# Performance work log

Hardware: AMD Instinct MI355X
Metric: run time of the kernel (lower is better)

The kernel has to match this reference:

```python
import jax, jax.numpy as jnp
import numpy as np

SIGMA = 1.0
T0, T1 = 0.0, 1.0
C, D = 8192, 3


def gram(x, y, sigma):
    # K(x, y) = exp(-||x - y||^2 / sigma^2), shape [N, M]
    x2 = jnp.sum(x * x, axis=-1)
    y2 = jnp.sum(y * y, axis=-1)
    d2 = x2[:, None] + y2[None, :] - 2.0 * (x @ y.T)
    return jnp.exp(-d2 / (sigma * sigma))


def setup_inputs() -> dict:
    key = jax.random.key(0)
    k1, k2 = jax.random.split(key)
    momentum = 0.01 * jax.random.normal(k1, (C, D), dtype=jnp.float32)
    control_points = jax.random.normal(k2, (C, D), dtype=jnp.float32)
    return {"momentum": momentum, "control_points": control_points, "steps": 5}


def reference(momentum, control_points, steps):
    sigma = SIGMA

    def hamiltonian(c, m):
        # H = 0.5 * sum(m * K(c, c) @ m)
        K = gram(c, c, sigma)
        return 0.5 * jnp.sum(m * (K @ m))

    def dyn(s):
        # Hamilton's equations: dc = dH/dm, dm = -dH/dc
        c, m = s[0], s[1]
        gc, gm = jax.grad(hamiltonian, argnums=(0, 1))(c, m)
        return jnp.stack([gm, -gc])

    t_span = jnp.linspace(T0, T1, steps)
    dt = (T1 - T0) / (steps - 1)
    s0 = jnp.stack([control_points, momentum])  # [2, C, d]

    def rk4_step(s, _):
        k1 = dyn(s)
        k2 = dyn(s + 0.5 * dt * k1)
        k3 = dyn(s + 0.5 * dt * k2)
        k4 = dyn(s + dt * k3)
        s_next = s + (dt / 6.0) * (k1 + 2.0 * k2 + 2.0 * k3 + k4)
        return s_next, s_next

    _, traj = jax.lax.scan(rk4_step, s0, None, length=steps - 1)
    st = jnp.concatenate([s0[None], traj], axis=0)  # [steps, 2, C, d]
    return t_span, st
```

## Files before the change

kernel.cpp:

```cpp
#include <hip/hip_runtime.h>


#define CN   8192
#define TPB  256
#define PTS  2
#define IGRP (TPB * PTS)
#define NIB  (CN / IGRP)
#define SJ   128
#define JC   (CN / SJ)
#define SSZ  (2 * CN * 3)

#define CSCALE 1.2011224087864498f
#define FSCALE (2.0f / CSCALE)


__global__ __launch_bounds__(TPB, 8) void dyn_kernel(
    const float* __restrict__ scur, const float* __restrict__ kprev,
    float coef, float* __restrict__ kout)
{
    __shared__ float4 jt[JC][2];
    const int tid = threadIdx.x;
    const int jbase = blockIdx.y * JC;

    {
        float* jf = (float*)jt;
#pragma unroll
        for (int q = tid; q < JC * 8; q += TPB) {
            const int p = jbase + (q >> 3), s = q & 7;
            float v = 0.f;
            if (s < 3) {
                v = (scur[p*3 + s] + coef * kprev[s*CN + p]) * CSCALE;
            } else if (s >= 4 && s < 7) {
                const int d = s - 4;
                v = scur[CN*3 + p*3 + d] + coef * kprev[(3 + d)*CN + p];
            }
            jf[q] = v;
        }
    }

    const int i0 = blockIdx.x * IGRP + tid;
    const int i1 = i0 + TPB;
    const float cx0 = (scur[i0*3+0] + coef*kprev[0*CN+i0]) * CSCALE;
    const float cy0 = (scur[i0*3+1] + coef*kprev[1*CN+i0]) * CSCALE;
    const float cz0 = (scur[i0*3+2] + coef*kprev[2*CN+i0]) * CSCALE;
    const float mx0 =  scur[CN*3+i0*3+0] + coef*kprev[3*CN+i0];
    const float my0 =  scur[CN*3+i0*3+1] + coef*kprev[4*CN+i0];
    const float mz0 =  scur[CN*3+i0*3+2] + coef*kprev[5*CN+i0];
    const float cx1 = (scur[i1*3+0] + coef*kprev[0*CN+i1]) * CSCALE;
    const float cy1 = (scur[i1*3+1] + coef*kprev[1*CN+i1]) * CSCALE;
    const float cz1 = (scur[i1*3+2] + coef*kprev[2*CN+i1]) * CSCALE;
    const float mx1 =  scur[CN*3+i1*3+0] + coef*kprev[3*CN+i1];
    const float my1 =  scur[CN*3+i1*3+1] + coef*kprev[4*CN+i1];
    const float mz1 =  scur[CN*3+i1*3+2] + coef*kprev[5*CN+i1];

    float gx0=0.f,gy0=0.f,gz0=0.f, fx0=0.f,fy0=0.f,fz0=0.f;
    float gx1=0.f,gy1=0.f,gz1=0.f, fx1=0.f,fy1=0.f,fz1=0.f;

    __syncthreads();

#pragma unroll 4
    for (int j = 0; j < JC; ++j) {
        const float4 A = jt[j][0];
        const float4 M = jt[j][1];
        {
            const float dx = cx0 - A.x, dy = cy0 - A.y, dz = cz0 - A.z;
            const float d2 = fmaf(dx, dx, fmaf(dy, dy, dz*dz));
            const float e  = __builtin_amdgcn_exp2f(-d2);
            const float md = fmaf(mx0, M.x, fmaf(my0, M.y, mz0 * M.z));
            const float w  = md * e;
            gx0 = fmaf(e, M.x, gx0); gy0 = fmaf(e, M.y, gy0); gz0 = fmaf(e, M.z, gz0);
            fx0 = fmaf(w, dx, fx0);  fy0 = fmaf(w, dy, fy0);  fz0 = fmaf(w, dz, fz0);
        }
        {
            const float dx = cx1 - A.x, dy = cy1 - A.y, dz = cz1 - A.z;
            const float d2 = fmaf(dx, dx, fmaf(dy, dy, dz*dz));
            const float e  = __builtin_amdgcn_exp2f(-d2);
            const float md = fmaf(mx1, M.x, fmaf(my1, M.y, mz1 * M.z));
            const float w  = md * e;
            gx1 = fmaf(e, M.x, gx1); gy1 = fmaf(e, M.y, gy1); gz1 = fmaf(e, M.z, gz1);
            fx1 = fmaf(w, dx, fx1);  fy1 = fmaf(w, dy, fy1);  fz1 = fmaf(w, dz, fz1);
        }
    }

    atomicAdd(&kout[0*CN+i0], gx0); atomicAdd(&kout[1*CN+i0], gy0); atomicAdd(&kout[2*CN+i0], gz0);
    atomicAdd(&kout[3*CN+i0], FSCALE*fx0); atomicAdd(&kout[4*CN+i0], FSCALE*fy0); atomicAdd(&kout[5*CN+i0], FSCALE*fz0);
    atomicAdd(&kout[0*CN+i1], gx1); atomicAdd(&kout[1*CN+i1], gy1); atomicAdd(&kout[2*CN+i1], gz1);
    atomicAdd(&kout[3*CN+i1], FSCALE*fx1); atomicAdd(&kout[4*CN+i1], FSCALE*fy1); atomicAdd(&kout[5*CN+i1], FSCALE*fz1);
}

__global__ __launch_bounds__(256) void advance_kernel(
    float* __restrict__ scur,
    float* __restrict__ k1, float* __restrict__ k2,
    float* __restrict__ k3, float* __restrict__ k4,
    float* __restrict__ outslot, float dt6)
{
    const int idx = blockIdx.x * 256 + threadIdx.x;
    if (idx >= 6 * CN) return;
    const int plane = idx >> 13, i = idx & (CN - 1);
    const int comp = (plane >= 3) ? 1 : 0, d = plane - comp * 3;
    const int off = comp * CN * 3 + i * 3 + d;
    const float v = scur[off] + dt6 * (k1[idx] + 2.f * (k2[idx] + k3[idx]) + k4[idx]);
    scur[off]    = v;
    outslot[off] = v;
    k1[idx] = 0.f; k2[idx] = 0.f; k3[idx] = 0.f; k4[idx] = 0.f;
}

__global__ __launch_bounds__(256) void init_kernel(
    const float* __restrict__ mom, const float* __restrict__ cp,
    float* __restrict__ out, float* __restrict__ scur,
    float* __restrict__ kb0, float* __restrict__ kb1,
    float* __restrict__ kb2, float* __restrict__ kb3)
{
    const int idx = blockIdx.x * 256 + threadIdx.x;
    if (idx < 5) out[idx] = 0.25f * (float)idx;
    if (idx < 6 * CN) { kb0[idx]=0.f; kb1[idx]=0.f; kb2[idx]=0.f; kb3[idx]=0.f; }
    if (idx < CN * 3) {
        const float cv = cp[idx], mv = mom[idx];
        scur[idx]          = cv;
        scur[CN * 3 + idx] = mv;
        out[5 + idx]            = cv;
        out[5 + CN * 3 + idx]   = mv;
    }
}

extern "C" void kernel_launch(void* const* d_in, const int* in_sizes, int n_in,
                              void* d_out, int out_size, void* d_ws, size_t ws_size,
                              hipStream_t stream)
{
    const float* mom = (const float*)d_in[0];
    const float* cp  = (const float*)d_in[1];
    float* out = (float*)d_out;
    float* ws  = (float*)d_ws;

    float* scur = ws;
    float* kb0  = ws + SSZ;
    float* kb1  = kb0 + 6 * CN;
    float* kb2  = kb1 + 6 * CN;
    float* kb3  = kb2 + 6 * CN;

    const float dt  = 0.25f;
    const float dt6 = dt / 6.f;

    init_kernel<<<(6 * CN + 255) / 256, 256, 0, stream>>>(mom, cp, out, scur,
                                                          kb0, kb1, kb2, kb3);
    dim3 dgrid(NIB, SJ);
    const int agrid = (6 * CN + 255) / 256;
    for (int step = 0; step < 4; ++step) {
        float* outslot = out + 5 + (size_t)(step + 1) * SSZ;
        dyn_kernel<<<dgrid, TPB, 0, stream>>>(scur, kb0, 0.0f,      kb0);
        dyn_kernel<<<dgrid, TPB, 0, stream>>>(scur, kb0, 0.5f * dt, kb1);
        dyn_kernel<<<dgrid, TPB, 0, stream>>>(scur, kb1, 0.5f * dt, kb2);
        dyn_kernel<<<dgrid, TPB, 0, stream>>>(scur, kb2, dt,        kb3);
        advance_kernel<<<agrid, 256, 0, stream>>>(scur, kb0, kb1, kb2, kb3, outslot, dt6);
    }
}
```

Baseline: 605.8 us.

## Expand distance algebraically and raise per-thread points to four

```diff
diff --git a/kernel.cpp b/kernel.cpp
--- a/kernel.cpp
+++ b/kernel.cpp
@@ -3,7 +3,7 @@
 
 #define CN   8192
 #define TPB  256
-#define PTS  2
+#define PTS  4
 #define IGRP (TPB * PTS)
 #define NIB  (CN / IGRP)
 #define SJ   128
@@ -13,8 +13,7 @@
 #define CSCALE 1.2011224087864498f
 #define FSCALE (2.0f / CSCALE)
 
-
-__global__ __launch_bounds__(TPB, 8) void dyn_kernel(
+__global__ __launch_bounds__(TPB, 4) void dyn_kernel(
     const float* __restrict__ scur, const float* __restrict__ kprev,
     float coef, float* __restrict__ kout)
 {
@@ -22,70 +21,66 @@
     const int tid = threadIdx.x;
     const int jbase = blockIdx.y * JC;
 
-    {
-        float* jf = (float*)jt;
+    if (tid < JC) {
+        const int p = jbase + tid;
+        const float sx = (scur[p*3+0] + coef * kprev[0*CN+p]) * CSCALE;
+        const float sy = (scur[p*3+1] + coef * kprev[1*CN+p]) * CSCALE;
+        const float sz = (scur[p*3+2] + coef * kprev[2*CN+p]) * CSCALE;
+        jt[tid][0] = make_float4(sx, sy, sz, fmaf(sx,sx, fmaf(sy,sy, sz*sz)));
+    } else if (tid < 2 * JC) {
+        const int p = jbase + tid - JC;
+        const float mx = scur[CN*3+p*3+0] + coef * kprev[3*CN+p];
+        const float my = scur[CN*3+p*3+1] + coef * kprev[4*CN+p];
+        const float mz = scur[CN*3+p*3+2] + coef * kprev[5*CN+p];
+        jt[tid - JC][1] = make_float4(mx, my, mz, 0.f);
+    }
+
+    float nx[PTS], ny[PTS], nz[PTS], c2[PTS];
+    float mx[PTS], my[PTS], mz[PTS];
+    float gx[PTS], gy[PTS], gz[PTS], hx[PTS], hy[PTS], hz[PTS], W[PTS];
 #pragma unroll
-        for (int q = tid; q < JC * 8; q += TPB) {
-            const int p = jbase + (q >> 3), s = q & 7;
-            float v = 0.f;
-            if (s < 3) {
-                v = (scur[p*3 + s] + coef * kprev[s*CN + p]) * CSCALE;
-            } else if (s >= 4 && s < 7) {
-                const int d = s - 4;
-                v = scur[CN*3 + p*3 + d] + coef * kprev[(3 + d)*CN + p];
-            }
-            jf[q] = v;
+    for (int q = 0; q < PTS; ++q) {
+        const int i = blockIdx.x * IGRP + tid + q * TPB;
+        const float cx = (scur[i*3+0] + coef * kprev[0*CN+i]) * CSCALE;
+        const float cy = (scur[i*3+1] + coef * kprev[1*CN+i]) * CSCALE;
+        const float cz = (scur[i*3+2] + coef * kprev[2*CN+i]) * CSCALE;
+        nx[q] = -2.f*cx; ny[q] = -2.f*cy; nz[q] = -2.f*cz;
+        c2[q] = fmaf(cx,cx, fmaf(cy,cy, cz*cz));
+        mx[q] = scur[CN*3+i*3+0] + coef * kprev[3*CN+i];
+        my[q] = scur[CN*3+i*3+1] + coef * kprev[4*CN+i];
+        mz[q] = scur[CN*3+i*3+2] + coef * kprev[5*CN+i];
+        gx[q]=0.f; gy[q]=0.f; gz[q]=0.f; hx[q]=0.f; hy[q]=0.f; hz[q]=0.f; W[q]=0.f;
+    }
+
+    __syncthreads();
+
+#pragma unroll 2
+    for (int j = 0; j < JC; ++j) {
+        const float4 A = jt[j][0];
+        const float4 M = jt[j][1];
+#pragma unroll
+        for (int q = 0; q < PTS; ++q) {
+            const float d2 = fmaf(nx[q], A.x, fmaf(ny[q], A.y, fmaf(nz[q], A.z, c2[q] + A.w)));
+            const float e  = __builtin_amdgcn_exp2f(-d2);
+            const float md = fmaf(mx[q], M.x, fmaf(my[q], M.y, mz[q] * M.z));
+            const float w  = md * e;
+            gx[q] = fmaf(e, M.x, gx[q]); gy[q] = fmaf(e, M.y, gy[q]); gz[q] = fmaf(e, M.z, gz[q]);
+            W[q] += w;
+            hx[q] = fmaf(w, A.x, hx[q]); hy[q] = fmaf(w, A.y, hy[q]); hz[q] = fmaf(w, A.z, hz[q]);
         }
     }
 
-    const int i0 = blockIdx.x * IGRP + tid;
-    const int i1 = i0 + TPB;
-    const float cx0 = (scur[i0*3+0] + coef*kprev[0*CN+i0]) * CSCALE;
-    const float cy0 = (scur[i0*3+1] + coef*kprev[1*CN+i0]) * CSCALE;
-    const float cz0 = (scur[i0*3+2] + coef*kprev[2*CN+i0]) * CSCALE;
-    const float mx0 =  scur[CN*3+i0*3+0] + coef*kprev[3*CN+i0];
-    const float my0 =  scur[CN*3+i0*3+1] + coef*kprev[4*CN+i0];
-    const float mz0 =  scur[CN*3+i0*3+2] + coef*kprev[5*CN+i0];
-    const float cx1 = (scur[i1*3+0] + coef*kprev[0*CN+i1]) * CSCALE;
-    const float cy1 = (scur[i1*3+1] + coef*kprev[1*CN+i1]) * CSCALE;
-    const float cz1 = (scur[i1*3+2] + coef*kprev[2*CN+i1]) * CSCALE;
-    const float mx1 =  scur[CN*3+i1*3+0] + coef*kprev[3*CN+i1];
-    const float my1 =  scur[CN*3+i1*3+1] + coef*kprev[4*CN+i1];
-    const float mz1 =  scur[CN*3+i1*3+2] + coef*kprev[5*CN+i1];
-
-    float gx0=0.f,gy0=0.f,gz0=0.f, fx0=0.f,fy0=0.f,fz0=0.f;
-    float gx1=0.f,gy1=0.f,gz1=0.f, fx1=0.f,fy1=0.f,fz1=0.f;
-
-    __syncthreads();
-
-#pragma unroll 4
-    for (int j = 0; j < JC; ++j) {
-        const float4 A = jt[j][0];
-        const float4 M = jt[j][1];
-        {
-            const float dx = cx0 - A.x, dy = cy0 - A.y, dz = cz0 - A.z;
-            const float d2 = fmaf(dx, dx, fmaf(dy, dy, dz*dz));
-            const float e  = __builtin_amdgcn_exp2f(-d2);
-            const float md = fmaf(mx0, M.x, fmaf(my0, M.y, mz0 * M.z));
-            const float w  = md * e;
-            gx0 = fmaf(e, M.x, gx0); gy0 = fmaf(e, M.y, gy0); gz0 = fmaf(e, M.z, gz0);
-            fx0 = fmaf(w, dx, fx0);  fy0 = fmaf(w, dy, fy0);  fz0 = fmaf(w, dz, fz0);
-        }
-        {
-            const float dx = cx1 - A.x, dy = cy1 - A.y, dz = cz1 - A.z;
-            const float d2 = fmaf(dx, dx, fmaf(dy, dy, dz*dz));
-            const float e  = __builtin_amdgcn_exp2f(-d2);
-            const float md = fmaf(mx1, M.x, fmaf(my1, M.y, mz1 * M.z));
-            const float w  = md * e;
-            gx1 = fmaf(e, M.x, gx1); gy1 = fmaf(e, M.y, gy1); gz1 = fmaf(e, M.z, gz1);
-            fx1 = fmaf(w, dx, fx1);  fy1 = fmaf(w, dy, fy1);  fz1 = fmaf(w, dz, fz1);
-        }
+#pragma unroll
+    for (int q = 0; q < PTS; ++q) {
+        const int i = blockIdx.x * IGRP + tid + q * TPB;
+        const float cx = -0.5f * nx[q], cy = -0.5f * ny[q], cz = -0.5f * nz[q];
+        atomicAdd(&kout[0*CN+i], gx[q]);
+        atomicAdd(&kout[1*CN+i], gy[q]);
+        atomicAdd(&kout[2*CN+i], gz[q]);
+        atomicAdd(&kout[3*CN+i], FSCALE * fmaf(cx, W[q], -hx[q]));
+        atomicAdd(&kout[4*CN+i], FSCALE * fmaf(cy, W[q], -hy[q]));
+        atomicAdd(&kout[5*CN+i], FSCALE * fmaf(cz, W[q], -hz[q]));
     }
-
-    atomicAdd(&kout[0*CN+i0], gx0); atomicAdd(&kout[1*CN+i0], gy0); atomicAdd(&kout[2*CN+i0], gz0);
-    atomicAdd(&kout[3*CN+i0], FSCALE*fx0); atomicAdd(&kout[4*CN+i0], FSCALE*fy0); atomicAdd(&kout[5*CN+i0], FSCALE*fz0);
-    atomicAdd(&kout[0*CN+i1], gx1); atomicAdd(&kout[1*CN+i1], gy1); atomicAdd(&kout[2*CN+i1], gz1);
-    atomicAdd(&kout[3*CN+i1], FSCALE*fx1); atomicAdd(&kout[4*CN+i1], FSCALE*fy1); atomicAdd(&kout[5*CN+i1], FSCALE*fz1);
 }
 
 __global__ __launch_bounds__(256) void advance_kernel(
@@ -147,7 +142,7 @@
     const int agrid = (6 * CN + 255) / 256;
     for (int step = 0; step < 4; ++step) {
         float* outslot = out + 5 + (size_t)(step + 1) * SSZ;
-        dyn_kernel<<<dgrid, TPB, 0, stream>>>(scur, kb0, 0.0f,      kb0);
+        dyn_kernel<<<dgrid, TPB, 0, stream>>>(scur, kb3, 0.0f,      kb0);
         dyn_kernel<<<dgrid, TPB, 0, stream>>>(scur, kb0, 0.5f * dt, kb1);
         dyn_kernel<<<dgrid, TPB, 0, stream>>>(scur, kb1, 0.5f * dt, kb2);
         dyn_kernel<<<dgrid, TPB, 0, stream>>>(scur, kb2, dt,        kb3);
```

Measured after the change: 589.5 us. 2.7% less time.
